# Kernel optimization log

Measured on AMD Instinct MI355X. Metric: run time of the kernel, lower is better.

## Reference

```python
import jax, jax.numpy as jnp
import numpy as np

BN_EPS = 1e-5

def batch_norm(x, gamma, beta):
    # training-mode BatchNorm1d: biased batch stats over the edge dim
    mean = jnp.mean(x, axis=0)
    var = jnp.var(x, axis=0)
    return (x - mean) * jax.lax.rsqrt(var + BN_EPS) * gamma + beta

def setup_inputs() -> dict:
    key = jax.random.key(0)
    ks = jax.random.split(key, 10)
    N, F, E = 50000, 128, 600000
    D_in = 2 * F + 12  # 268
    h = jax.random.normal(ks[0], (N, F), dtype=jnp.float32)
    edge_feature = jax.random.normal(ks[1], (E, 12), dtype=jnp.float32)
    src = jax.random.randint(ks[2], (E,), 0, N)
    dst = jax.random.randint(ks[3], (E,), 0, N)
    def lin(k, fan_in, shape):
        bound = 1.0 / np.sqrt(fan_in)
        return jax.random.uniform(k, shape, jnp.float32, -bound, bound)
    W1 = lin(ks[4], D_in, (28, D_in)); b1 = lin(ks[5], D_in, (28,))
    W2 = lin(ks[6], 28, (8, 28));      b2 = lin(ks[7], 28, (8,))
    W3 = lin(ks[8], 8, (1, 8));        b3 = lin(ks[9], 8, (1,))
    gamma1 = jnp.ones((28,), jnp.float32); beta1 = jnp.zeros((28,), jnp.float32)
    gamma2 = jnp.ones((8,), jnp.float32);  beta2 = jnp.zeros((8,), jnp.float32)
    return {"h": h, "edge_feature": edge_feature, "src": src, "dst": dst,
            "W1": W1, "b1": b1, "gamma1": gamma1, "beta1": beta1,
            "W2": W2, "b2": b2, "gamma2": gamma2, "beta2": beta2,
            "W3": W3, "b3": b3}

def reference(h, edge_feature, src, dst, W1, b1, gamma1, beta1,
              W2, b2, gamma2, beta2, W3, b3):
    h_u = h[src]                    # [E, F] gather of source node feats
    h_v = h[dst]                    # [E, F] gather of dest node feats
    x = jnp.concatenate([h_u, h_v, edge_feature], axis=1)  # [E, 2F+12]
    s = jax.nn.relu(batch_norm(x @ W1.T + b1, gamma1, beta1))  # [E, 28]
    s = jax.nn.relu(batch_norm(s @ W2.T + b2, gamma2, beta2))  # [E, 8]
    score = s @ W3.T + b3           # [E, 1]
    return score
```

## Files before the change

### kernel.cpp

```cpp
#include <hip/hip_runtime.h>

#define BN_EPS 1e-5f


__global__ void k1_proj(const float* __restrict__ h, const float* __restrict__ W1,
                        float* __restrict__ Psrc, float* __restrict__ Pdst,
                        float* __restrict__ stats, int N) {
  __shared__ float lwk[3584];
  if (blockIdx.x == 0 && threadIdx.x < 72) stats[threadIdx.x] = 0.f;
  const int half = blockIdx.x & 1;
  for (int j = threadIdx.x * 4; j < 3584; j += 1024) {
    const int c = j >> 7, k = j & 127;
    *(float4*)&lwk[j] = *(const float4*)(W1 + c * 268 + half * 128 + k);
  }
  __syncthreads();
  const int node = (blockIdx.x >> 1) * 256 + threadIdx.x;
  if (node >= N) return;

  const float4* __restrict__ h4 = (const float4*)(h + (size_t)node * 128);
  float acc[28];
#pragma unroll
  for (int c = 0; c < 28; c++) acc[c] = 0.f;

  for (int kk = 0; kk < 16; kk++) {
    const float4 a = h4[kk * 2];
    const float4 b = h4[kk * 2 + 1];
#pragma unroll
    for (int c = 0; c < 28; c++) {
      const float4 w0 = *(const float4*)&lwk[c * 128 + kk * 8];
      const float4 w1 = *(const float4*)&lwk[c * 128 + kk * 8 + 4];
      acc[c] += a.x * w0.x + a.y * w0.y + a.z * w0.z + a.w * w0.w
              + b.x * w1.x + b.y * w1.y + b.z * w1.z + b.w * w1.w;
    }
  }

  float4* po = (float4*)((half ? Pdst : Psrc) + (size_t)node * 32);
#pragma unroll
  for (int q = 0; q < 7; q++) {
    po[q] = make_float4(acc[q * 4], acc[q * 4 + 1], acc[q * 4 + 2], acc[q * 4 + 3]);
  }
  po[7] = make_float4(0.f, 0.f, 0.f, 0.f);
}

__global__ __launch_bounds__(256)
void k2_edge(const float* __restrict__ Psrc, const float* __restrict__ Pdst,
             const float* __restrict__ ef,
             const int* __restrict__ src, const int* __restrict__ dst,
             const float* __restrict__ W1, const float* __restrict__ b1,
             float* __restrict__ y1, float* __restrict__ stats, int E) {
  __shared__ float lw[28][12];
  __shared__ float lb[28];
  __shared__ float tile[7168];
  __shared__ float lsum[8][28], lssq[8][28];
  const int tid = threadIdx.x;
  for (int i = tid; i < 336; i += 256) lw[i / 12][i % 12] = W1[(i / 12) * 268 + 256 + (i % 12)];
  if (tid < 28) lb[tid] = b1[tid];
  if (tid < 224) { lsum[tid / 28][tid % 28] = 0.f; lssq[tid / 28][tid % 28] = 0.f; }
  __syncthreads();

  float sx = 0.f, sy = 0.f, sz = 0.f, sw = 0.f;
  float qx = 0.f, qy = 0.f, qz = 0.f, qw = 0.f;

  for (int t = 0; t < 2; t++) {
    const int base = (blockIdx.x * 2 + t) * 256;
    const int e = base + tid;
    if (e < E) {
      const int s = src[e], d = dst[e];
      const float4* __restrict__ pa4 = (const float4*)(Psrc + (size_t)s * 32);
      const float4* __restrict__ pb4 = (const float4*)(Pdst + (size_t)d * 32);
      const float4* __restrict__ e4 = (const float4*)(ef + (size_t)e * 12);
      float f[12];
#pragma unroll
      for (int q = 0; q < 3; q++) {
        const float4 v = e4[q];
        f[q * 4] = v.x; f[q * 4 + 1] = v.y; f[q * 4 + 2] = v.z; f[q * 4 + 3] = v.w;
      }
      float* tr = &tile[tid * 28];
#pragma unroll
      for (int q = 0; q < 7; q++) {
        const float4 ta = pa4[q];
        const float4 tb = pb4[q];
        float vv[4];
#pragma unroll
        for (int i2 = 0; i2 < 4; i2++) {
          const int c = q * 4 + i2;
          const float4* lw4 = (const float4*)(&lw[c][0]);
          const float4 w0 = lw4[0], w1 = lw4[1], w2 = lw4[2];
          vv[i2] = lb[c]
              + f[0] * w0.x + f[1] * w0.y + f[2] * w0.z + f[3] * w0.w
              + f[4] * w1.x + f[5] * w1.y + f[6] * w1.z + f[7] * w1.w
              + f[8] * w2.x + f[9] * w2.y + f[10] * w2.z + f[11] * w2.w;
        }
        *(float4*)&tr[q * 4] = make_float4(vv[0] + ta.x + tb.x, vv[1] + ta.y + tb.y,
                                           vv[2] + ta.z + tb.z, vv[3] + ta.w + tb.w);
      }
    }
    __syncthreads();
    const int nval = min(256, E - base) * 28;
    if (tid < 224) {
      const size_t gbase = (size_t)base * 28;
#pragma unroll
      for (int i = 0; i < 8; i++) {
        const int jl = tid * 4 + i * 896;
        if (jl < nval) {
          const float4 v = *(const float4*)&tile[jl];
          *(float4*)(y1 + gbase + jl) = v;
          sx += v.x; sy += v.y; sz += v.z; sw += v.w;
          qx += v.x * v.x; qy += v.y * v.y; qz += v.z * v.z; qw += v.w * v.w;
        }
      }
    }
    __syncthreads();
  }

  if (tid < 224) {
    const int c0 = (tid * 4) % 28, a8 = tid / 28;
    atomicAdd(&lsum[a8][c0], sx);     atomicAdd(&lssq[a8][c0], qx);
    atomicAdd(&lsum[a8][c0 + 1], sy); atomicAdd(&lssq[a8][c0 + 1], qy);
    atomicAdd(&lsum[a8][c0 + 2], sz); atomicAdd(&lssq[a8][c0 + 2], qz);
    atomicAdd(&lsum[a8][c0 + 3], sw); atomicAdd(&lssq[a8][c0 + 3], qw);
  }
  __syncthreads();
  if (tid < 28) {
    float S = 0.f, Q = 0.f;
#pragma unroll
    for (int a = 0; a < 8; a++) { S += lsum[a][tid]; Q += lssq[a][tid]; }
    atomicAdd(&stats[tid], S);
    atomicAdd(&stats[28 + tid], Q);
  }
}

__global__ void k3_fin1(const float* __restrict__ gamma, const float* __restrict__ beta,
                        float* __restrict__ stats, float invE) {
  const int c = threadIdx.x;
  if (c < 28) {
    const float mean = stats[c] * invE;
    const float var = stats[28 + c] * invE - mean * mean;
    const float sc = gamma[c] * rsqrtf(var + BN_EPS);
    stats[72 + c] = sc;
    stats[100 + c] = beta[c] - mean * sc;
  }
}

__global__ void k4_l2(const float* __restrict__ y1, const float* __restrict__ statsRO,
                      const float* __restrict__ W2, const float* __restrict__ b2,
                      float* __restrict__ y2, float* __restrict__ statsW, int E) {
  __shared__ float tile[7168];
  __shared__ float4 w2q[8][7];
  __shared__ float4 scq[7], shq[7];
  __shared__ float lb2[8];
  const int tid = threadIdx.x;
  if (tid < 56) {
    w2q[tid / 7][tid % 7] = *(const float4*)(W2 + (tid / 7) * 28 + (tid % 7) * 4);
  } else if (tid < 63) {
    const int q = tid - 56;
    scq[q] = *(const float4*)(statsRO + 72 + q * 4);
    shq[q] = *(const float4*)(statsRO + 100 + q * 4);
  } else if (tid >= 64 && tid < 72) {
    lb2[tid - 64] = b2[tid - 64];
  }
  float as[8], aq[8];
#pragma unroll
  for (int o = 0; o < 8; o++) { as[o] = 0.f; aq[o] = 0.f; }

  for (int t = 0; t < 2; t++) {
    const int base = (blockIdx.x * 2 + t) * 256;
    const int nval = min(256, E - base) * 28;
    __syncthreads();
    if (tid < 224) {
      const size_t gbase = (size_t)base * 28;
#pragma unroll
      for (int i = 0; i < 8; i++) {
        const int jl = tid * 4 + i * 896;
        if (jl < nval) *(float4*)&tile[jl] = *(const float4*)(y1 + gbase + jl);
      }
    }
    __syncthreads();
    const int e = base + tid;
    if (e < E) {
      float accv[8];
#pragma unroll
      for (int o = 0; o < 8; o++) accv[o] = lb2[o];
      const float* tr = &tile[tid * 28];
#pragma unroll
      for (int q = 0; q < 7; q++) {
        const float4 sv = *(const float4*)&tr[q * 4];
        const float4 sc = scq[q], sh = shq[q];
        const float s0 = fmaxf(sv.x * sc.x + sh.x, 0.f);
        const float s1 = fmaxf(sv.y * sc.y + sh.y, 0.f);
        const float s2 = fmaxf(sv.z * sc.z + sh.z, 0.f);
        const float s3 = fmaxf(sv.w * sc.w + sh.w, 0.f);
#pragma unroll
        for (int o = 0; o < 8; o++) {
          const float4 w = w2q[o][q];
          accv[o] += s0 * w.x + s1 * w.y + s2 * w.z + s3 * w.w;
        }
      }
      float4* yo = (float4*)(y2 + (size_t)e * 8);
      yo[0] = make_float4(accv[0], accv[1], accv[2], accv[3]);
      yo[1] = make_float4(accv[4], accv[5], accv[6], accv[7]);
#pragma unroll
      for (int o = 0; o < 8; o++) { as[o] += accv[o]; aq[o] += accv[o] * accv[o]; }
    }
  }

#pragma unroll
  for (int o = 0; o < 8; o++) {
    for (int off = 32; off; off >>= 1) {
      as[o] += __shfl_down(as[o], off);
      aq[o] += __shfl_down(aq[o], off);
    }
  }
  __shared__ float redS[4][16];
  const int wave = tid >> 6, lane = tid & 63;
  if (lane == 0) {
#pragma unroll
    for (int o = 0; o < 8; o++) { redS[wave][o] = as[o]; redS[wave][8 + o] = aq[o]; }
  }
  __syncthreads();
  if (tid < 16) {
    atomicAdd(&statsW[56 + tid], redS[0][tid] + redS[1][tid] + redS[2][tid] + redS[3][tid]);
  }
}

__global__ void k5_fin2(const float* __restrict__ gamma, const float* __restrict__ beta,
                        float* __restrict__ stats, float invE) {
  const int c = threadIdx.x;
  if (c < 8) {
    const float mean = stats[56 + c] * invE;
    const float var = stats[64 + c] * invE - mean * mean;
    const float sc = gamma[c] * rsqrtf(var + BN_EPS);
    stats[128 + c] = sc;
    stats[136 + c] = beta[c] - mean * sc;
  }
}

__global__ void k6_l3(const float* __restrict__ y2, const float* __restrict__ stats,
                      const float* __restrict__ W3, const float* __restrict__ b3,
                      float* __restrict__ out, int E) {
  const int e = blockIdx.x * blockDim.x + threadIdx.x;
  if (e >= E) return;
  const float4* p = (const float4*)(y2 + (size_t)e * 8);
  float4 a = p[0], b4 = p[1];
  float v[8] = {a.x, a.y, a.z, a.w, b4.x, b4.y, b4.z, b4.w};
  float acc = b3[0];
#pragma unroll
  for (int o = 0; o < 8; o++) {
    float s = fmaxf(v[o] * stats[128 + o] + stats[136 + o], 0.f);
    acc += W3[o] * s;
  }
  out[e] = acc;
}

extern "C" void kernel_launch(void* const* d_in, const int* in_sizes, int n_in,
                              void* d_out, int out_size, void* d_ws, size_t ws_size,
                              hipStream_t stream) {
  const float* h   = (const float*)d_in[0];
  const float* ef  = (const float*)d_in[1];
  const int* src   = (const int*)d_in[2];
  const int* dst   = (const int*)d_in[3];
  const float* W1  = (const float*)d_in[4];
  const float* b1  = (const float*)d_in[5];
  const float* g1  = (const float*)d_in[6];
  const float* be1 = (const float*)d_in[7];
  const float* W2  = (const float*)d_in[8];
  const float* b2  = (const float*)d_in[9];
  const float* g2  = (const float*)d_in[10];
  const float* be2 = (const float*)d_in[11];
  const float* W3  = (const float*)d_in[12];
  const float* b3  = (const float*)d_in[13];
  float* out = (float*)d_out;

  const int N = in_sizes[0] / 128;
  const int E = in_sizes[2];
  const float invE = 1.0f / (float)E;

  float* ws = (float*)d_ws;
  float* stats = ws;
  float* Psrc = ws + 256;
  float* y1 = Psrc + (size_t)N * 32;
  float* y2 = y1 + (size_t)E * 28;
  float* Pdst = y2;

  const int nodeBlocks = (N + 255) / 256;
  const int nTiles = (E + 255) / 256;
  const int nPair = (nTiles + 1) / 2;
  k1_proj<<<nodeBlocks * 2, 256, 0, stream>>>(h, W1, Psrc, Pdst, stats, N);
  k2_edge<<<nPair, 256, 0, stream>>>(Psrc, Pdst, ef, src, dst, W1, b1, y1, stats, E);
  k3_fin1<<<1, 32, 0, stream>>>(g1, be1, stats, invE);
  k4_l2<<<nPair, 256, 0, stream>>>(y1, stats, W2, b2, y2, stats, E);
  k5_fin2<<<1, 64, 0, stream>>>(g2, be2, stats, invE);
  k6_l3<<<nTiles, 256, 0, stream>>>(y2, stats, W3, b3, out, E);
}
```

Before: 260.0 us.

## Fold BN finalize kernels into consumers and use one tile per edge block

Removes the two single-block BatchNorm finalize kernels by having each consumer block compute the scale and shift from the accumulated sums in shared memory, which cuts two launches and their serialization gaps. The edge kernel now processes one 256-edge tile per block instead of two, doubling the grid and halving per-block work. In exchange there are twice as many global stats atomics in the edge kernel, and every consumer block recomputes the same scale/shift.

```diff
diff --git a/kernel.cpp b/kernel.cpp
--- a/kernel.cpp
+++ b/kernel.cpp
@@ -61,56 +61,53 @@
   float sx = 0.f, sy = 0.f, sz = 0.f, sw = 0.f;
   float qx = 0.f, qy = 0.f, qz = 0.f, qw = 0.f;
 
-  for (int t = 0; t < 2; t++) {
-    const int base = (blockIdx.x * 2 + t) * 256;
-    const int e = base + tid;
-    if (e < E) {
-      const int s = src[e], d = dst[e];
-      const float4* __restrict__ pa4 = (const float4*)(Psrc + (size_t)s * 32);
-      const float4* __restrict__ pb4 = (const float4*)(Pdst + (size_t)d * 32);
-      const float4* __restrict__ e4 = (const float4*)(ef + (size_t)e * 12);
-      float f[12];
-#pragma unroll
-      for (int q = 0; q < 3; q++) {
-        const float4 v = e4[q];
-        f[q * 4] = v.x; f[q * 4 + 1] = v.y; f[q * 4 + 2] = v.z; f[q * 4 + 3] = v.w;
-      }
-      float* tr = &tile[tid * 28];
-#pragma unroll
-      for (int q = 0; q < 7; q++) {
-        const float4 ta = pa4[q];
-        const float4 tb = pb4[q];
-        float vv[4];
-#pragma unroll
-        for (int i2 = 0; i2 < 4; i2++) {
-          const int c = q * 4 + i2;
-          const float4* lw4 = (const float4*)(&lw[c][0]);
-          const float4 w0 = lw4[0], w1 = lw4[1], w2 = lw4[2];
-          vv[i2] = lb[c]
-              + f[0] * w0.x + f[1] * w0.y + f[2] * w0.z + f[3] * w0.w
-              + f[4] * w1.x + f[5] * w1.y + f[6] * w1.z + f[7] * w1.w
-              + f[8] * w2.x + f[9] * w2.y + f[10] * w2.z + f[11] * w2.w;
-        }
-        *(float4*)&tr[q * 4] = make_float4(vv[0] + ta.x + tb.x, vv[1] + ta.y + tb.y,
-                                           vv[2] + ta.z + tb.z, vv[3] + ta.w + tb.w);
-      }
-    }
-    __syncthreads();
-    const int nval = min(256, E - base) * 28;
-    if (tid < 224) {
-      const size_t gbase = (size_t)base * 28;
-#pragma unroll
-      for (int i = 0; i < 8; i++) {
-        const int jl = tid * 4 + i * 896;
-        if (jl < nval) {
-          const float4 v = *(const float4*)&tile[jl];
-          *(float4*)(y1 + gbase + jl) = v;
-          sx += v.x; sy += v.y; sz += v.z; sw += v.w;
-          qx += v.x * v.x; qy += v.y * v.y; qz += v.z * v.z; qw += v.w * v.w;
-        }
-      }
-    }
-    __syncthreads();
+  const int base = blockIdx.x * 256;
+  const int e = base + tid;
+  if (e < E) {
+    const int s = src[e], d = dst[e];
+    const float4* __restrict__ pa4 = (const float4*)(Psrc + (size_t)s * 32);
+    const float4* __restrict__ pb4 = (const float4*)(Pdst + (size_t)d * 32);
+    const float4* __restrict__ e4 = (const float4*)(ef + (size_t)e * 12);
+    float f[12];
+#pragma unroll
+    for (int q = 0; q < 3; q++) {
+      const float4 v = e4[q];
+      f[q * 4] = v.x; f[q * 4 + 1] = v.y; f[q * 4 + 2] = v.z; f[q * 4 + 3] = v.w;
+    }
+    float* tr = &tile[tid * 28];
+#pragma unroll
+    for (int q = 0; q < 7; q++) {
+      const float4 ta = pa4[q];
+      const float4 tb = pb4[q];
+      float vv[4];
+#pragma unroll
+      for (int i2 = 0; i2 < 4; i2++) {
+        const int c = q * 4 + i2;
+        const float4* lw4 = (const float4*)(&lw[c][0]);
+        const float4 w0 = lw4[0], w1 = lw4[1], w2 = lw4[2];
+        vv[i2] = lb[c]
+            + f[0] * w0.x + f[1] * w0.y + f[2] * w0.z + f[3] * w0.w
+            + f[4] * w1.x + f[5] * w1.y + f[6] * w1.z + f[7] * w1.w
+            + f[8] * w2.x + f[9] * w2.y + f[10] * w2.z + f[11] * w2.w;
+      }
+      *(float4*)&tr[q * 4] = make_float4(vv[0] + ta.x + tb.x, vv[1] + ta.y + tb.y,
+                                         vv[2] + ta.z + tb.z, vv[3] + ta.w + tb.w);
+    }
+  }
+  __syncthreads();
+  const int nval = min(256, E - base) * 28;
+  if (tid < 224) {
+    const size_t gbase = (size_t)base * 28;
+#pragma unroll
+    for (int i = 0; i < 8; i++) {
+      const int jl = tid * 4 + i * 896;
+      if (jl < nval) {
+        const float4 v = *(const float4*)&tile[jl];
+        *(float4*)(y1 + gbase + jl) = v;
+        sx += v.x; sy += v.y; sz += v.z; sw += v.w;
+        qx += v.x * v.x; qy += v.y * v.y; qz += v.z * v.z; qw += v.w * v.w;
+      }
+    }
   }
 
   if (tid < 224) {
@@ -130,34 +127,27 @@
   }
 }
 
-__global__ void k3_fin1(const float* __restrict__ gamma, const float* __restrict__ beta,
-                        float* __restrict__ stats, float invE) {
-  const int c = threadIdx.x;
-  if (c < 28) {
-    const float mean = stats[c] * invE;
-    const float var = stats[28 + c] * invE - mean * mean;
-    const float sc = gamma[c] * rsqrtf(var + BN_EPS);
-    stats[72 + c] = sc;
-    stats[100 + c] = beta[c] - mean * sc;
-  }
-}
-
 __global__ void k4_l2(const float* __restrict__ y1, const float* __restrict__ statsRO,
                       const float* __restrict__ W2, const float* __restrict__ b2,
-                      float* __restrict__ y2, float* __restrict__ statsW, int E) {
+                      const float* __restrict__ g1, const float* __restrict__ be1,
+                      float* __restrict__ y2, float* __restrict__ statsW,
+                      int E, float invE) {
   __shared__ float tile[7168];
   __shared__ float4 w2q[8][7];
-  __shared__ float4 scq[7], shq[7];
+  __shared__ float scs[28], shs[28];
   __shared__ float lb2[8];
   const int tid = threadIdx.x;
   if (tid < 56) {
     w2q[tid / 7][tid % 7] = *(const float4*)(W2 + (tid / 7) * 28 + (tid % 7) * 4);
-  } else if (tid < 63) {
-    const int q = tid - 56;
-    scq[q] = *(const float4*)(statsRO + 72 + q * 4);
-    shq[q] = *(const float4*)(statsRO + 100 + q * 4);
-  } else if (tid >= 64 && tid < 72) {
-    lb2[tid - 64] = b2[tid - 64];
+  } else if (tid >= 64 && tid < 92) {
+    const int c = tid - 64;
+    const float mean = statsRO[c] * invE;
+    const float var = statsRO[28 + c] * invE - mean * mean;
+    const float sc = g1[c] * rsqrtf(var + BN_EPS);
+    scs[c] = sc;
+    shs[c] = be1[c] - mean * sc;
+  } else if (tid >= 96 && tid < 104) {
+    lb2[tid - 96] = b2[tid - 96];
   }
   float as[8], aq[8];
 #pragma unroll
@@ -185,7 +175,8 @@
 #pragma unroll
       for (int q = 0; q < 7; q++) {
         const float4 sv = *(const float4*)&tr[q * 4];
-        const float4 sc = scq[q], sh = shq[q];
+        const float4 sc = *(const float4*)&scs[q * 4];
+        const float4 sh = *(const float4*)&shs[q * 4];
         const float s0 = fmaxf(sv.x * sc.x + sh.x, 0.f);
         const float s1 = fmaxf(sv.y * sc.y + sh.y, 0.f);
         const float s2 = fmaxf(sv.z * sc.z + sh.z, 0.f);
@@ -223,31 +214,33 @@
   }
 }
 
-__global__ void k5_fin2(const float* __restrict__ gamma, const float* __restrict__ beta,
-                        float* __restrict__ stats, float invE) {
-  const int c = threadIdx.x;
-  if (c < 8) {
+__global__ void k6_l3(const float* __restrict__ y2, const float* __restrict__ stats,
+                      const float* __restrict__ g2, const float* __restrict__ be2,
+                      const float* __restrict__ W3, const float* __restrict__ b3,
+                      float* __restrict__ out, int E, float invE) {
+  __shared__ float sc2[8], sh2[8], w3[8];
+  __shared__ float b3s;
+  if (threadIdx.x < 8) {
+    const int c = threadIdx.x;
     const float mean = stats[56 + c] * invE;
     const float var = stats[64 + c] * invE - mean * mean;
-    const float sc = gamma[c] * rsqrtf(var + BN_EPS);
-    stats[128 + c] = sc;
-    stats[136 + c] = beta[c] - mean * sc;
-  }
-}
-
-__global__ void k6_l3(const float* __restrict__ y2, const float* __restrict__ stats,
-                      const float* __restrict__ W3, const float* __restrict__ b3,
-                      float* __restrict__ out, int E) {
+    const float sc = g2[c] * rsqrtf(var + BN_EPS);
+    sc2[c] = sc;
+    sh2[c] = be2[c] - mean * sc;
+    w3[c] = W3[c];
+    if (c == 0) b3s = b3[0];
+  }
+  __syncthreads();
   const int e = blockIdx.x * blockDim.x + threadIdx.x;
   if (e >= E) return;
   const float4* p = (const float4*)(y2 + (size_t)e * 8);
   float4 a = p[0], b4 = p[1];
   float v[8] = {a.x, a.y, a.z, a.w, b4.x, b4.y, b4.z, b4.w};
-  float acc = b3[0];
+  float acc = b3s;
 #pragma unroll
   for (int o = 0; o < 8; o++) {
-    float s = fmaxf(v[o] * stats[128 + o] + stats[136 + o], 0.f);
-    acc += W3[o] * s;
+    float s = fmaxf(v[o] * sc2[o] + sh2[o], 0.f);
+    acc += w3[o] * s;
   }
   out[e] = acc;
 }
@@ -286,9 +279,7 @@
   const int nTiles = (E + 255) / 256;
   const int nPair = (nTiles + 1) / 2;
   k1_proj<<<nodeBlocks * 2, 256, 0, stream>>>(h, W1, Psrc, Pdst, stats, N);
-  k2_edge<<<nPair, 256, 0, stream>>>(Psrc, Pdst, ef, src, dst, W1, b1, y1, stats, E);
-  k3_fin1<<<1, 32, 0, stream>>>(g1, be1, stats, invE);
-  k4_l2<<<nPair, 256, 0, stream>>>(y1, stats, W2, b2, y2, stats, E);
-  k5_fin2<<<1, 64, 0, stream>>>(g2, be2, stats, invE);
-  k6_l3<<<nTiles, 256, 0, stream>>>(y2, stats, W3, b3, out, E);
-}
+  k2_edge<<<nTiles, 256, 0, stream>>>(Psrc, Pdst, ef, src, dst, W1, b1, y1, stats, E);
+  k4_l2<<<nPair, 256, 0, stream>>>(y1, stats, W2, b2, g1, be1, y2, stats, E, invE);
+  k6_l3<<<nTiles, 256, 0, stream>>>(y2, stats, g2, be2, W3, b3, out, E, invE);
+}
```

New measurement: 282.9 us. 8.8% more time.
